# Kernel optimization log

Measured on AMD Instinct MI355X. Metric: run time of the kernel, lower is better.

## Reference

```python
import jax, jax.numpy as jnp
import numpy as np

D_MODEL = 1024
NUM_HEADS = 16
HEAD_DIM = D_MODEL // NUM_HEADS
BATCH = 2
SEQ = 2048


def setup_inputs() -> dict:
    key = jax.random.key(0)
    ks = jax.random.split(key, 9)
    s_in = 1.0 / np.sqrt(D_MODEL)  # kaiming-ish fan-in scaling for stability
    return {
        "x": jax.random.normal(ks[0], (BATCH, SEQ, D_MODEL), jnp.float32),
        "wq": jax.random.normal(ks[1], (D_MODEL, D_MODEL), jnp.float32) * s_in,
        "bq": jnp.zeros((D_MODEL,), jnp.float32),
        "wk": jax.random.normal(ks[2], (D_MODEL, D_MODEL), jnp.float32) * s_in,
        "bk": jnp.zeros((D_MODEL,), jnp.float32),
        "wv": jax.random.normal(ks[3], (D_MODEL, D_MODEL), jnp.float32) * s_in,
        "bv": jnp.zeros((D_MODEL,), jnp.float32),
        "wo": jax.random.normal(ks[4], (D_MODEL, D_MODEL), jnp.float32) * s_in,
        "bo": jnp.zeros((D_MODEL,), jnp.float32),
    }


def reference(x, wq, bq, wk, bk, wv, bv, wo, bo):
    B, S, _ = x.shape
    # QKV projections, split heads: [B, H, S, Dh]
    def proj(w, b):
        y = x @ w + b
        return y.reshape(B, S, NUM_HEADS, HEAD_DIM).transpose(0, 2, 1, 3)

    q = proj(wq, bq)
    k = proj(wk, bk)
    v = proj(wv, bv)

    scale = 1.0 / jnp.sqrt(jnp.float32(HEAD_DIM))
    scores = jnp.einsum("bhsd,bhtd->bhst", q, k) * scale  # [B,H,S,S]
    attn = jax.nn.softmax(scores, axis=-1)
    out = jnp.einsum("bhst,bhtd->bhsd", attn, v)  # [B,H,S,Dh]
    out = out.transpose(0, 2, 1, 3).reshape(B, S, D_MODEL)
    return out @ wo + bo
```

## Files before the change

kernel.cpp:

```cpp
#include <hip/hip_runtime.h>
#include <stdint.h>
#include <stddef.h>


typedef __attribute__((ext_vector_type(8))) short short8;
typedef __attribute__((ext_vector_type(4))) float f32x4;
typedef __attribute__((ext_vector_type(16))) float f32x16;
typedef __attribute__((ext_vector_type(4))) unsigned short u16x4;

#define MFMA16(a, b, c) __builtin_amdgcn_mfma_f32_16x16x32_bf16((a), (b), (c), 0, 0, 0)
#define MFMA32(a, b, c) __builtin_amdgcn_mfma_f32_32x32x16_bf16((a), (b), (c), 0, 0, 0)
#define AS1 __attribute__((address_space(1)))
#define AS3 __attribute__((address_space(3)))

__device__ __forceinline__ unsigned short f2bf(float f) {
  union { float f; unsigned u; } v; v.f = f;
  unsigned r = v.u + 0x7fffu + ((v.u >> 16) & 1u);
  return (unsigned short)(r >> 16);
}

__device__ __forceinline__ unsigned cvt_pk_bf16(float lo, float hi) {
  unsigned r;
  asm("v_cvt_pk_bf16_f32 %0, %1, %2" : "=v"(r) : "v"(lo), "v"(hi));
  return r;
}

__device__ __forceinline__ void pl32_swap(unsigned& a, unsigned& b) {
  asm volatile("v_permlane32_swap_b32 %0, %1" : "+v"(a), "+v"(b));
}

__device__ __forceinline__ short8 mk8(unsigned a, unsigned b, unsigned c, unsigned d) {
  union { unsigned u[4]; short8 s; } v;
  v.u[0] = a; v.u[1] = b; v.u[2] = c; v.u[3] = d;
  return v.s;
}

__global__ __launch_bounds__(256) void cast_x_kernel(const float* __restrict__ x,
                                                     unsigned short* __restrict__ xb) {
  int i = (blockIdx.x * 256 + threadIdx.x) * 4;
  float4 v = *reinterpret_cast<const float4*>(x + i);
  u16x4 o;
  o.x = f2bf(v.x); o.y = f2bf(v.y); o.z = f2bf(v.z); o.w = f2bf(v.w);
  *reinterpret_cast<u16x4*>(xb + i) = o;
}

__global__ __launch_bounds__(256) void prep_w_kernel(const float* __restrict__ wq,
                                                     const float* __restrict__ wk,
                                                     const float* __restrict__ wv,
                                                     const float* __restrict__ wo,
                                                     unsigned short* __restrict__ wt) {
  __shared__ unsigned short t_lds[32][33];
  int bid = blockIdx.x;
  int wsel = bid >> 10;
  int rem = bid & 1023;
  int kb = (rem >> 5) << 5;
  int nb = (rem & 31) << 5;
  const float* W = (wsel == 0) ? wq : (wsel == 1) ? wk : (wsel == 2) ? wv : wo;
  int t = threadIdx.x;
  int r = t >> 3, c = (t & 7) * 4;
  float4 v = *reinterpret_cast<const float4*>(W + (size_t)(kb + r) * 1024 + nb + c);
  t_lds[r][c + 0] = f2bf(v.x);
  t_lds[r][c + 1] = f2bf(v.y);
  t_lds[r][c + 2] = f2bf(v.z);
  t_lds[r][c + 3] = f2bf(v.w);
  __syncthreads();
  u16x4 o;
  o.x = t_lds[c + 0][r]; o.y = t_lds[c + 1][r];
  o.z = t_lds[c + 2][r]; o.w = t_lds[c + 3][r];
  *reinterpret_cast<u16x4*>(wt + (size_t)(wsel * 1024 + nb + r) * 1024 + kb + c) = o;
}

__global__ __launch_bounds__(256) void pack_bias_kernel(const float* __restrict__ bq,
                                                        const float* __restrict__ bk,
                                                        const float* __restrict__ bv,
                                                        float* __restrict__ bias3) {
  int i = blockIdx.x * 256 + threadIdx.x;
  if (i < 3072) bias3[i] = (i < 1024) ? bq[i] : (i < 2048) ? bk[i - 1024] : bv[i - 2048];
}

template <typename OutT, bool QS>
__global__ __launch_bounds__(256) void gemm_bt_kernel(const unsigned short* __restrict__ A,
                                                      const unsigned short* __restrict__ Bt,
                                                      const float* __restrict__ bias,
                                                      OutT* __restrict__ C, int N) {
  constexpr int K = 1024;
  __shared__ __align__(16) unsigned short a_lds[2][128 * 32];
  __shared__ __align__(16) unsigned short b_lds[2][128 * 32];
  const int nb = N >> 7;
  const int nwg = nb << 5;
  const int cpx = nwg >> 3;
  const int wg = ((int)blockIdx.x & 7) * cpx + ((int)blockIdx.x >> 3);
  const int bm = wg / nb;
  const int bn = wg % nb;
  const int m0 = bm << 7, n0 = bn << 7;
  const int tid = threadIdx.x;
  const int w = tid >> 6, l = tid & 63;
  const int lr = l & 15, lg = l >> 4;
  const int wm = (w >> 1) << 6, wn = (w & 1) << 6;

  const int q0 = w * 2, q1 = w * 2 + 1;
  const unsigned short* pa0 = A + (size_t)(m0 + q0 * 16 + (l >> 2)) * K + (l & 3) * 8;
  const unsigned short* pa1 = A + (size_t)(m0 + q1 * 16 + (l >> 2)) * K + (l & 3) * 8;
  const unsigned short* pb0 = Bt + (size_t)(n0 + q0 * 16 + (l >> 2)) * K + (l & 3) * 8;
  const unsigned short* pb1 = Bt + (size_t)(n0 + q1 * 16 + (l >> 2)) * K + (l & 3) * 8;

#define GEMM_STAGE(buf, k0)                                                        \
  do {                                                                             \
    __builtin_amdgcn_global_load_lds((const AS1 void*)(pa0 + (k0)),                \
        (AS3 void*)(&a_lds[buf][q0 * 512]), 16, 0, 0);                             \
    __builtin_amdgcn_global_load_lds((const AS1 void*)(pa1 + (k0)),                \
        (AS3 void*)(&a_lds[buf][q1 * 512]), 16, 0, 0);                             \
    __builtin_amdgcn_global_load_lds((const AS1 void*)(pb0 + (k0)),                \
        (AS3 void*)(&b_lds[buf][q0 * 512]), 16, 0, 0);                             \
    __builtin_amdgcn_global_load_lds((const AS1 void*)(pb1 + (k0)),                \
        (AS3 void*)(&b_lds[buf][q1 * 512]), 16, 0, 0);                             \
  } while (0)

  f32x4 acc[4][4] = {};
  GEMM_STAGE(0, 0);
  __syncthreads();

  int cur = 0;
  for (int k0 = 0; k0 < K; k0 += 32) {
    if (k0 + 32 < K) GEMM_STAGE(cur ^ 1, k0 + 32);
    short8 af[4], bfr[4];
#pragma unroll
    for (int i = 0; i < 4; ++i)
      af[i] = *reinterpret_cast<const short8*>(&a_lds[cur][(wm + i * 16 + lr) * 32 + lg * 8]);
#pragma unroll
    for (int i = 0; i < 4; ++i)
      bfr[i] = *reinterpret_cast<const short8*>(&b_lds[cur][(wn + i * 16 + lr) * 32 + lg * 8]);
#pragma unroll
    for (int i = 0; i < 4; ++i)
#pragma unroll
      for (int j = 0; j < 4; ++j)
        acc[i][j] = MFMA16(af[i], bfr[j], acc[i][j]);
    __syncthreads();
    cur ^= 1;
  }
#undef GEMM_STAGE

  const float scale = (QS && n0 < 1024) ? 0.18033688011111f : 1.0f;
#pragma unroll
  for (int i = 0; i < 4; ++i) {
#pragma unroll
    for (int j = 0; j < 4; ++j) {
#pragma unroll
      for (int r = 0; r < 4; ++r) {
        int m = m0 + wm + i * 16 + lg * 4 + r;
        int n = n0 + wn + j * 16 + lr;
        float val = (acc[i][j][r] + bias[n]) * scale;
        if constexpr (sizeof(OutT) == 2) {
          C[(size_t)m * N + n] = (OutT)f2bf(val);
        } else {
          C[(size_t)m * N + n] = val;
        }
      }
    }
  }
}

__global__ __launch_bounds__(256) void attn_kernel(const unsigned short* __restrict__ qkv,
                                                   unsigned short* __restrict__ aout) {
  __shared__ __align__(16) char lds[32768];
  const int tid = threadIdx.x;
  const int w = tid >> 6, l = tid & 63;
  const int lq = l & 31, hi = l >> 5;
  const int wg = ((int)blockIdx.x & 7) * 64 + ((int)blockIdx.x >> 3);
  const int qblk = wg & 15;
  const int bh = wg >> 4;
  const int b = bh >> 4, h = bh & 15;
  const size_t rowbase = (size_t)b * 2048;
  const int q0 = qblk * 128 + w * 32;

  short8 qf[4];
  {
    const unsigned short* qrow = qkv + (rowbase + q0 + lq) * 3072 + h * 64 + hi * 8;
#pragma unroll
    for (int c = 0; c < 4; ++c)
      qf[c] = *reinterpret_cast<const short8*>(qrow + c * 16);
  }

  const int r0 = 16 * w + (l >> 3);
  const int r1 = r0 + 8;
  const char* kq0_src = (const char*)(qkv + rowbase * 3072 + 1024 + h * 64) +
                        (size_t)r0 * 6144 + ((16 * (l & 7)) ^ ((r0 & 6) << 4));
  const char* kq1_src = (const char*)(qkv + rowbase * 3072 + 1024 + h * 64) +
                        (size_t)r1 * 6144 + ((16 * (l & 7)) ^ ((r1 & 6) << 4));
  const int kdst0 = 2 * w * 1024;
  const int kdst1 = kdst0 + 1024;

  const int pi = tid & 31;
  const int vd0 = (tid >> 5) * 8;
  const unsigned short* vptr_a = qkv + (rowbase + 2 * pi) * 3072 + 2048 + h * 64 + vd0;
  const unsigned short* vptr_b = vptr_a + 3072;

  int aoff[4];
#pragma unroll
  for (int c = 0; c < 4; ++c)
    aoff[c] = lq * 128 + ((c * 32 + hi * 16) ^ ((lq & 6) << 4));
  int vwoff[4];
#pragma unroll
  for (int jr = 0; jr < 4; ++jr)
    vwoff[jr] = 16384 + (vd0 + 2 * jr) * 128 + ((4 * pi) ^ ((2 * jr) << 4));

  float ls0 = 0.f, ls1 = 0.f, ls2 = 0.f, ls3 = 0.f;
  f32x16 ot0 = {}, ot1 = {};

  __builtin_amdgcn_global_load_lds((const AS1 void*)kq0_src, (AS3 void*)(lds + kdst0), 16, 0, 0);
  __builtin_amdgcn_global_load_lds((const AS1 void*)kq1_src, (AS3 void*)(lds + kdst1), 16, 0, 0);
  kq0_src += 393216; kq1_src += 393216;
  {
    short8 va = *reinterpret_cast<const short8*>(vptr_a);
    short8 vb = *reinterpret_cast<const short8*>(vptr_b);
    vptr_a += 64 * 3072; vptr_b += 64 * 3072;
    union { short8 s; unsigned u[4]; } ua, ub;
    ua.s = va; ub.s = vb;
#pragma unroll
    for (int jr = 0; jr < 4; ++jr) {
      unsigned w0 = __builtin_amdgcn_perm(ub.u[jr], ua.u[jr], 0x05040100u);
      unsigned w1 = __builtin_amdgcn_perm(ub.u[jr], ua.u[jr], 0x07060302u);
      *reinterpret_cast<unsigned*>(lds + vwoff[jr]) = w0;
      *reinterpret_cast<unsigned*>(lds + vwoff[jr] + 128) = w1;
    }
  }
  __syncthreads();

  int cur = 0;
  for (int t0 = 0; t0 < 2048; t0 += 64) {
    const bool more = (t0 + 64) < 2048;
    const int bmask = cur << 13;
    const int nmask = bmask ^ 8192;
    short8 va, vb;
    if (more) {
      __builtin_amdgcn_global_load_lds((const AS1 void*)kq0_src,
                                       (AS3 void*)(lds + nmask + kdst0), 16, 0, 0);
      __builtin_amdgcn_global_load_lds((const AS1 void*)kq1_src,
                                       (AS3 void*)(lds + nmask + kdst1), 16, 0, 0);
      kq0_src += 393216; kq1_src += 393216;
      va = *reinterpret_cast<const short8*>(vptr_a);
      vb = *reinterpret_cast<const short8*>(vptr_b);
      vptr_a += 64 * 3072; vptr_b += 64 * 3072;
    }

    const char* fb0 = lds + (aoff[0] ^ bmask);
    const char* fb1 = lds + (aoff[1] ^ bmask);
    const char* fb2 = lds + (aoff[2] ^ bmask);
    const char* fb3 = lds + (aoff[3] ^ bmask);

    f32x16 s0 = {}, s1 = {};
    __builtin_amdgcn_s_setprio(1);
    s0 = MFMA32(*reinterpret_cast<const short8*>(fb0), qf[0], s0);
    s1 = MFMA32(*reinterpret_cast<const short8*>(fb0 + 4096), qf[0], s1);
    s0 = MFMA32(*reinterpret_cast<const short8*>(fb1), qf[1], s0);
    s1 = MFMA32(*reinterpret_cast<const short8*>(fb1 + 4096), qf[1], s1);
    s0 = MFMA32(*reinterpret_cast<const short8*>(fb2), qf[2], s0);
    s1 = MFMA32(*reinterpret_cast<const short8*>(fb2 + 4096), qf[2], s1);
    s0 = MFMA32(*reinterpret_cast<const short8*>(fb3), qf[3], s0);
    s1 = MFMA32(*reinterpret_cast<const short8*>(fb3 + 4096), qf[3], s1);
    __builtin_amdgcn_s_setprio(0);

    if (more) {
      union { short8 s; unsigned u[4]; } ua, ub;
      ua.s = va; ub.s = vb;
#pragma unroll
      for (int jr = 0; jr < 4; ++jr) {
        unsigned w0 = __builtin_amdgcn_perm(ub.u[jr], ua.u[jr], 0x05040100u);
        unsigned w1 = __builtin_amdgcn_perm(ub.u[jr], ua.u[jr], 0x07060302u);
        *reinterpret_cast<unsigned*>(lds + (vwoff[jr] ^ nmask) - 16384 + 16384) = w0;
        *reinterpret_cast<unsigned*>(lds + (vwoff[jr] ^ nmask) + 128) = w1;
      }
    }

    float p0[16], p1[16];
#pragma unroll
    for (int i = 0; i < 16; ++i) {
      p0[i] = __builtin_exp2f(s0[i]);
      if ((i & 3) == 0) ls0 += p0[i]; else if ((i & 3) == 1) ls1 += p0[i];
      else if ((i & 3) == 2) ls2 += p0[i]; else ls3 += p0[i];
    }
#pragma unroll
    for (int i = 0; i < 16; ++i) {
      p1[i] = __builtin_exp2f(s1[i]);
      if ((i & 3) == 0) ls0 += p1[i]; else if ((i & 3) == 1) ls1 += p1[i];
      else if ((i & 3) == 2) ls2 += p1[i]; else ls3 += p1[i];
    }

    short8 pf[4];
    {
      unsigned a0 = cvt_pk_bf16(p0[0], p0[1]),   a1 = cvt_pk_bf16(p0[4], p0[5]);
      unsigned b0 = cvt_pk_bf16(p0[2], p0[3]),   b1 = cvt_pk_bf16(p0[6], p0[7]);
      pl32_swap(a0, a1); pl32_swap(b0, b1);
      pf[0] = mk8(a0, b0, a1, b1);
      unsigned c0 = cvt_pk_bf16(p0[8], p0[9]),   c1 = cvt_pk_bf16(p0[12], p0[13]);
      unsigned d0 = cvt_pk_bf16(p0[10], p0[11]), d1 = cvt_pk_bf16(p0[14], p0[15]);
      pl32_swap(c0, c1); pl32_swap(d0, d1);
      pf[1] = mk8(c0, d0, c1, d1);
      unsigned e0 = cvt_pk_bf16(p1[0], p1[1]),   e1 = cvt_pk_bf16(p1[4], p1[5]);
      unsigned f0 = cvt_pk_bf16(p1[2], p1[3]),   f1 = cvt_pk_bf16(p1[6], p1[7]);
      pl32_swap(e0, e1); pl32_swap(f0, f1);
      pf[2] = mk8(e0, f0, e1, f1);
      unsigned g0 = cvt_pk_bf16(p1[8], p1[9]),   g1 = cvt_pk_bf16(p1[12], p1[13]);
      unsigned h0 = cvt_pk_bf16(p1[10], p1[11]), h1 = cvt_pk_bf16(p1[14], p1[15]);
      pl32_swap(g0, g1); pl32_swap(h0, h1);
      pf[3] = mk8(g0, h0, g1, h1);
    }

    __builtin_amdgcn_s_setprio(1);
    ot0 = MFMA32(*reinterpret_cast<const short8*>(fb0 + 16384), pf[0], ot0);
    ot1 = MFMA32(*reinterpret_cast<const short8*>(fb0 + 20480), pf[0], ot1);
    ot0 = MFMA32(*reinterpret_cast<const short8*>(fb1 + 16384), pf[1], ot0);
    ot1 = MFMA32(*reinterpret_cast<const short8*>(fb1 + 20480), pf[1], ot1);
    ot0 = MFMA32(*reinterpret_cast<const short8*>(fb2 + 16384), pf[2], ot0);
    ot1 = MFMA32(*reinterpret_cast<const short8*>(fb2 + 20480), pf[2], ot1);
    ot0 = MFMA32(*reinterpret_cast<const short8*>(fb3 + 16384), pf[3], ot0);
    ot1 = MFMA32(*reinterpret_cast<const short8*>(fb3 + 20480), pf[3], ot1);
    __builtin_amdgcn_s_setprio(0);

    __syncthreads();
    cur ^= 1;
  }

  float lsum = (ls0 + ls1) + (ls2 + ls3);
  lsum += __shfl_xor(lsum, 32, 64);
  const float inv = 1.0f / lsum;
  char* ob = lds + w * 4096;
  const int swz_lq = (lq & 6) << 4;
#pragma unroll
  for (int r = 0; r < 16; r += 2) {
    int d = (r & 3) + 8 * (r >> 2) + 4 * hi;
    unsigned pk0 = cvt_pk_bf16(ot0[r] * inv, ot0[r + 1] * inv);
    *(unsigned*)(ob + lq * 128 + ((2 * d) ^ swz_lq)) = pk0;
    unsigned pk1 = cvt_pk_bf16(ot1[r] * inv, ot1[r + 1] * inv);
    *(unsigned*)(ob + lq * 128 + ((2 * (32 + d)) ^ swz_lq)) = pk1;
  }
  __syncthreads();
#pragma unroll
  for (int it = 0; it < 4; ++it) {
    int qq = it * 32 + (tid >> 3);
    int ch = tid & 7;
    const char* src = lds + (qq >> 5) * 4096;
    short8 vv = *reinterpret_cast<const short8*>(
        src + (qq & 31) * 128 + ((ch * 16) ^ (((qq & 31) & 6) << 4)));
    *reinterpret_cast<short8*>(aout + (rowbase + qblk * 128 + qq) * 1024 + h * 64 + ch * 8) = vv;
  }
}

extern "C" void kernel_launch(void* const* d_in, const int* in_sizes, int n_in,
                              void* d_out, int out_size, void* d_ws, size_t ws_size,
                              hipStream_t stream) {
  const float* x  = (const float*)d_in[0];
  const float* wq = (const float*)d_in[1];
  const float* bq = (const float*)d_in[2];
  const float* wk = (const float*)d_in[3];
  const float* bk = (const float*)d_in[4];
  const float* wv = (const float*)d_in[5];
  const float* bv = (const float*)d_in[6];
  const float* wo = (const float*)d_in[7];
  const float* bo = (const float*)d_in[8];
  float* out = (float*)d_out;

  char* ws = (char*)d_ws;
  unsigned short* xb    = (unsigned short*)(ws);
  unsigned short* aob   = (unsigned short*)(ws);
  unsigned short* wt    = (unsigned short*)(ws + 8388608);
  float*          bias3 = (float*)(ws + 16777216);
  unsigned short* qkvb  = (unsigned short*)(ws + 16777216 + 16384);

  cast_x_kernel<<<4096, 256, 0, stream>>>(x, xb);
  prep_w_kernel<<<4096, 256, 0, stream>>>(wq, wk, wv, wo, wt);
  pack_bias_kernel<<<12, 256, 0, stream>>>(bq, bk, bv, bias3);

  gemm_bt_kernel<unsigned short, true><<<768, 256, 0, stream>>>(xb, wt, bias3, qkvb, 3072);

  attn_kernel<<<512, 256, 0, stream>>>(qkvb, aob);

  gemm_bt_kernel<float, false><<<256, 256, 0, stream>>>(aob, wt + (size_t)3072 * 1024, bo, out, 1024);
}
```

Baseline: 141.3 us.

## Write V transposed from QKV GEMM and split attention keys across waves

The QKV projection epilogue now writes Q and K into a 2048-wide buffer and V in a pre-transposed [b,h,d,s] layout. This removes the in-kernel permute and LDS staging of V in attention. The attention kernel drops LDS double buffering and reads K and V fragments straight from global memory. It uses 128-thread blocks over 32 query rows, where each of the two waves handles half the keys, and merges the partial outputs and row sums through LDS at the end. The change aims for more parallelism and less LDS and sync traffic, at the cost of uncoalesced strided global loads of K and direct global V reads with no explicit prefetch.

```diff
diff --git a/kernel.cpp b/kernel.cpp
--- a/kernel.cpp
+++ b/kernel.cpp
@@ -78,11 +78,14 @@
   if (i < 3072) bias3[i] = (i < 1024) ? bq[i] : (i < 2048) ? bk[i - 1024] : bv[i - 2048];
 }
 
-template <typename OutT, bool QS>
+template <int MODE>
 __global__ __launch_bounds__(256) void gemm_bt_kernel(const unsigned short* __restrict__ A,
                                                       const unsigned short* __restrict__ Bt,
                                                       const float* __restrict__ bias,
-                                                      OutT* __restrict__ C, int N) {
+                                                      float* __restrict__ Cf,
+                                                      unsigned short* __restrict__ qk,
+                                                      unsigned short* __restrict__ vt,
+                                                      int N) {
   constexpr int K = 1024;
   __shared__ __align__(16) unsigned short a_lds[2][128 * 32];
   __shared__ __align__(16) unsigned short b_lds[2][128 * 32];
@@ -140,137 +143,94 @@
   }
 #undef GEMM_STAGE
 
-  const float scale = (QS && n0 < 1024) ? 0.18033688011111f : 1.0f;
-#pragma unroll
-  for (int i = 0; i < 4; ++i) {
-#pragma unroll
-    for (int j = 0; j < 4; ++j) {
-#pragma unroll
-      for (int r = 0; r < 4; ++r) {
-        int m = m0 + wm + i * 16 + lg * 4 + r;
-        int n = n0 + wn + j * 16 + lr;
-        float val = (acc[i][j][r] + bias[n]) * scale;
-        if constexpr (sizeof(OutT) == 2) {
-          C[(size_t)m * N + n] = (OutT)f2bf(val);
-        } else {
-          C[(size_t)m * N + n] = val;
+  if constexpr (MODE == 0) {
+#pragma unroll
+    for (int i = 0; i < 4; ++i)
+#pragma unroll
+      for (int j = 0; j < 4; ++j)
+#pragma unroll
+        for (int r = 0; r < 4; ++r) {
+          int m = m0 + wm + i * 16 + lg * 4 + r;
+          int n = n0 + wn + j * 16 + lr;
+          Cf[(size_t)m * N + n] = acc[i][j][r] + bias[n];
+        }
+  } else {
+    if (n0 < 2048) {
+      const float scale = (n0 < 1024) ? 0.18033688011111f : 1.0f;
+#pragma unroll
+      for (int i = 0; i < 4; ++i)
+#pragma unroll
+        for (int j = 0; j < 4; ++j)
+#pragma unroll
+          for (int r = 0; r < 4; ++r) {
+            int m = m0 + wm + i * 16 + lg * 4 + r;
+            int n = n0 + wn + j * 16 + lr;
+            qk[(size_t)m * 2048 + n] = f2bf((acc[i][j][r] + bias[n]) * scale);
+          }
+    } else {
+#pragma unroll
+      for (int i = 0; i < 4; ++i) {
+        int m_ = m0 + wm + i * 16 + lg * 4;
+        int bb = m_ >> 11, ss = m_ & 2047;
+#pragma unroll
+        for (int j = 0; j < 4; ++j) {
+          int np = n0 - 2048 + wn + j * 16 + lr;
+          int hh = np >> 6, dd = np & 63;
+          float bv = bias[np + 2048];
+          u16x4 pk;
+          pk.x = f2bf(acc[i][j][0] + bv);
+          pk.y = f2bf(acc[i][j][1] + bv);
+          pk.z = f2bf(acc[i][j][2] + bv);
+          pk.w = f2bf(acc[i][j][3] + bv);
+          *reinterpret_cast<u16x4*>(vt + (size_t)(bb * 16 + hh) * 131072 + dd * 2048 + ss) = pk;
         }
       }
     }
   }
 }
 
-__global__ __launch_bounds__(256) void attn_kernel(const unsigned short* __restrict__ qkv,
-                                                   unsigned short* __restrict__ aout) {
-  __shared__ __align__(16) char lds[32768];
+__global__ __launch_bounds__(128, 4) void attn_kernel(const unsigned short* __restrict__ qk,
+                                                      const unsigned short* __restrict__ vt,
+                                                      unsigned short* __restrict__ aout) {
+  __shared__ __align__(16) char lds[12544];
   const int tid = threadIdx.x;
   const int w = tid >> 6, l = tid & 63;
   const int lq = l & 31, hi = l >> 5;
-  const int wg = ((int)blockIdx.x & 7) * 64 + ((int)blockIdx.x >> 3);
-  const int qblk = wg & 15;
-  const int bh = wg >> 4;
+  const int wg = ((int)blockIdx.x & 7) * 256 + ((int)blockIdx.x >> 3);
+  const int bh = wg >> 6, qb = wg & 63;
   const int b = bh >> 4, h = bh & 15;
-  const size_t rowbase = (size_t)b * 2048;
-  const int q0 = qblk * 128 + w * 32;
 
   short8 qf[4];
   {
-    const unsigned short* qrow = qkv + (rowbase + q0 + lq) * 3072 + h * 64 + hi * 8;
+    const unsigned short* qrow = qk + (size_t)(b * 2048 + qb * 32 + lq) * 2048 + h * 64 + hi * 8;
 #pragma unroll
     for (int c = 0; c < 4; ++c)
       qf[c] = *reinterpret_cast<const short8*>(qrow + c * 16);
   }
 
-  const int r0 = 16 * w + (l >> 3);
-  const int r1 = r0 + 8;
-  const char* kq0_src = (const char*)(qkv + rowbase * 3072 + 1024 + h * 64) +
-                        (size_t)r0 * 6144 + ((16 * (l & 7)) ^ ((r0 & 6) << 4));
-  const char* kq1_src = (const char*)(qkv + rowbase * 3072 + 1024 + h * 64) +
-                        (size_t)r1 * 6144 + ((16 * (l & 7)) ^ ((r1 & 6) << 4));
-  const int kdst0 = 2 * w * 1024;
-  const int kdst1 = kdst0 + 1024;
-
-  const int pi = tid & 31;
-  const int vd0 = (tid >> 5) * 8;
-  const unsigned short* vptr_a = qkv + (rowbase + 2 * pi) * 3072 + 2048 + h * 64 + vd0;
-  const unsigned short* vptr_b = vptr_a + 3072;
-
-  int aoff[4];
-#pragma unroll
-  for (int c = 0; c < 4; ++c)
-    aoff[c] = lq * 128 + ((c * 32 + hi * 16) ^ ((lq & 6) << 4));
-  int vwoff[4];
-#pragma unroll
-  for (int jr = 0; jr < 4; ++jr)
-    vwoff[jr] = 16384 + (vd0 + 2 * jr) * 128 + ((4 * pi) ^ ((2 * jr) << 4));
+  const unsigned short* kp =
+      qk + (size_t)(b * 2048 + w * 1024 + lq) * 2048 + 1024 + h * 64 + hi * 8;
+  const unsigned short* vp = vt + (size_t)bh * 131072 + (size_t)lq * 2048 + w * 1024 + hi * 8;
 
   float ls0 = 0.f, ls1 = 0.f, ls2 = 0.f, ls3 = 0.f;
   f32x16 ot0 = {}, ot1 = {};
 
-  __builtin_amdgcn_global_load_lds((const AS1 void*)kq0_src, (AS3 void*)(lds + kdst0), 16, 0, 0);
-  __builtin_amdgcn_global_load_lds((const AS1 void*)kq1_src, (AS3 void*)(lds + kdst1), 16, 0, 0);
-  kq0_src += 393216; kq1_src += 393216;
-  {
-    short8 va = *reinterpret_cast<const short8*>(vptr_a);
-    short8 vb = *reinterpret_cast<const short8*>(vptr_b);
-    vptr_a += 64 * 3072; vptr_b += 64 * 3072;
-    union { short8 s; unsigned u[4]; } ua, ub;
-    ua.s = va; ub.s = vb;
-#pragma unroll
-    for (int jr = 0; jr < 4; ++jr) {
-      unsigned w0 = __builtin_amdgcn_perm(ub.u[jr], ua.u[jr], 0x05040100u);
-      unsigned w1 = __builtin_amdgcn_perm(ub.u[jr], ua.u[jr], 0x07060302u);
-      *reinterpret_cast<unsigned*>(lds + vwoff[jr]) = w0;
-      *reinterpret_cast<unsigned*>(lds + vwoff[jr] + 128) = w1;
-    }
-  }
-  __syncthreads();
-
-  int cur = 0;
-  for (int t0 = 0; t0 < 2048; t0 += 64) {
-    const bool more = (t0 + 64) < 2048;
-    const int bmask = cur << 13;
-    const int nmask = bmask ^ 8192;
-    short8 va, vb;
-    if (more) {
-      __builtin_amdgcn_global_load_lds((const AS1 void*)kq0_src,
-                                       (AS3 void*)(lds + nmask + kdst0), 16, 0, 0);
-      __builtin_amdgcn_global_load_lds((const AS1 void*)kq1_src,
-                                       (AS3 void*)(lds + nmask + kdst1), 16, 0, 0);
-      kq0_src += 393216; kq1_src += 393216;
-      va = *reinterpret_cast<const short8*>(vptr_a);
-      vb = *reinterpret_cast<const short8*>(vptr_b);
-      vptr_a += 64 * 3072; vptr_b += 64 * 3072;
-    }
-
-    const char* fb0 = lds + (aoff[0] ^ bmask);
-    const char* fb1 = lds + (aoff[1] ^ bmask);
-    const char* fb2 = lds + (aoff[2] ^ bmask);
-    const char* fb3 = lds + (aoff[3] ^ bmask);
+  for (int it = 0; it < 16; ++it) {
+    short8 vta[4];
+#pragma unroll
+    for (int c = 0; c < 4; ++c)
+      vta[c] = *reinterpret_cast<const short8*>(vp + c * 16);
 
     f32x16 s0 = {}, s1 = {};
     __builtin_amdgcn_s_setprio(1);
-    s0 = MFMA32(*reinterpret_cast<const short8*>(fb0), qf[0], s0);
-    s1 = MFMA32(*reinterpret_cast<const short8*>(fb0 + 4096), qf[0], s1);
-    s0 = MFMA32(*reinterpret_cast<const short8*>(fb1), qf[1], s0);
-    s1 = MFMA32(*reinterpret_cast<const short8*>(fb1 + 4096), qf[1], s1);
-    s0 = MFMA32(*reinterpret_cast<const short8*>(fb2), qf[2], s0);
-    s1 = MFMA32(*reinterpret_cast<const short8*>(fb2 + 4096), qf[2], s1);
-    s0 = MFMA32(*reinterpret_cast<const short8*>(fb3), qf[3], s0);
-    s1 = MFMA32(*reinterpret_cast<const short8*>(fb3 + 4096), qf[3], s1);
+#pragma unroll
+    for (int c = 0; c < 4; ++c) {
+      short8 kf0 = *reinterpret_cast<const short8*>(kp + c * 16);
+      short8 kf1 = *reinterpret_cast<const short8*>(kp + 32 * 2048 + c * 16);
+      s0 = MFMA32(kf0, qf[c], s0);
+      s1 = MFMA32(kf1, qf[c], s1);
+    }
     __builtin_amdgcn_s_setprio(0);
-
-    if (more) {
-      union { short8 s; unsigned u[4]; } ua, ub;
-      ua.s = va; ub.s = vb;
-#pragma unroll
-      for (int jr = 0; jr < 4; ++jr) {
-        unsigned w0 = __builtin_amdgcn_perm(ub.u[jr], ua.u[jr], 0x05040100u);
-        unsigned w1 = __builtin_amdgcn_perm(ub.u[jr], ua.u[jr], 0x07060302u);
-        *reinterpret_cast<unsigned*>(lds + (vwoff[jr] ^ nmask) - 16384 + 16384) = w0;
-        *reinterpret_cast<unsigned*>(lds + (vwoff[jr] ^ nmask) + 128) = w1;
-      }
-    }
 
     float p0[16], p1[16];
 #pragma unroll
@@ -307,42 +267,60 @@
     }
 
     __builtin_amdgcn_s_setprio(1);
-    ot0 = MFMA32(*reinterpret_cast<const short8*>(fb0 + 16384), pf[0], ot0);
-    ot1 = MFMA32(*reinterpret_cast<const short8*>(fb0 + 20480), pf[0], ot1);
-    ot0 = MFMA32(*reinterpret_cast<const short8*>(fb1 + 16384), pf[1], ot0);
-    ot1 = MFMA32(*reinterpret_cast<const short8*>(fb1 + 20480), pf[1], ot1);
-    ot0 = MFMA32(*reinterpret_cast<const short8*>(fb2 + 16384), pf[2], ot0);
-    ot1 = MFMA32(*reinterpret_cast<const short8*>(fb2 + 20480), pf[2], ot1);
-    ot0 = MFMA32(*reinterpret_cast<const short8*>(fb3 + 16384), pf[3], ot0);
-    ot1 = MFMA32(*reinterpret_cast<const short8*>(fb3 + 20480), pf[3], ot1);
+#pragma unroll
+    for (int c = 0; c < 4; ++c) {
+      short8 vtb = *reinterpret_cast<const short8*>(vp + 32 * 2048 + c * 16);
+      ot0 = MFMA32(vta[c], pf[c], ot0);
+      ot1 = MFMA32(vtb, pf[c], ot1);
+    }
     __builtin_amdgcn_s_setprio(0);
 
-    __syncthreads();
-    cur ^= 1;
-  }
+    kp += 64 * 2048;
+    vp += 64;
+  }
+
+  float* mbuf = (float*)lds;
+  float* dbuf = (float*)(lds + 8192);
+  char*  obuf = lds + 8320;
 
   float lsum = (ls0 + ls1) + (ls2 + ls3);
   lsum += __shfl_xor(lsum, 32, 64);
-  const float inv = 1.0f / lsum;
-  char* ob = lds + w * 4096;
-  const int swz_lq = (lq & 6) << 4;
-#pragma unroll
-  for (int r = 0; r < 16; r += 2) {
-    int d = (r & 3) + 8 * (r >> 2) + 4 * hi;
-    unsigned pk0 = cvt_pk_bf16(ot0[r] * inv, ot0[r + 1] * inv);
-    *(unsigned*)(ob + lq * 128 + ((2 * d) ^ swz_lq)) = pk0;
-    unsigned pk1 = cvt_pk_bf16(ot1[r] * inv, ot1[r + 1] * inv);
-    *(unsigned*)(ob + lq * 128 + ((2 * (32 + d)) ^ swz_lq)) = pk1;
+
+  if (w == 1) {
+#pragma unroll
+    for (int r = 0; r < 16; ++r) {
+      int d = (r & 3) + 8 * (r >> 2) + 4 * hi;
+      mbuf[d * 32 + lq] = ot0[r];
+      mbuf[(32 + d) * 32 + lq] = ot1[r];
+    }
+    if (hi == 0) dbuf[lq] = lsum;
   }
   __syncthreads();
-#pragma unroll
-  for (int it = 0; it < 4; ++it) {
-    int qq = it * 32 + (tid >> 3);
-    int ch = tid & 7;
-    const char* src = lds + (qq >> 5) * 4096;
-    short8 vv = *reinterpret_cast<const short8*>(
-        src + (qq & 31) * 128 + ((ch * 16) ^ (((qq & 31) & 6) << 4)));
-    *reinterpret_cast<short8*>(aout + (rowbase + qblk * 128 + qq) * 1024 + h * 64 + ch * 8) = vv;
+  if (w == 0) {
+    const float inv = 1.0f / (lsum + dbuf[lq]);
+    const int swz = (lq & 7) << 4;
+#pragma unroll
+    for (int r = 0; r < 16; r += 2) {
+      int d = (r & 3) + 8 * (r >> 2) + 4 * hi;
+      float o0a = (ot0[r] + mbuf[d * 32 + lq]) * inv;
+      float o0b = (ot0[r + 1] + mbuf[(d + 1) * 32 + lq]) * inv;
+      *(unsigned*)(obuf + lq * 128 + ((2 * d) ^ swz)) = cvt_pk_bf16(o0a, o0b);
+      float o1a = (ot1[r] + mbuf[(32 + d) * 32 + lq]) * inv;
+      float o1b = (ot1[r + 1] + mbuf[(33 + d) * 32 + lq]) * inv;
+      *(unsigned*)(obuf + lq * 128 + ((2 * (32 + d)) ^ swz)) = cvt_pk_bf16(o1a, o1b);
+    }
+  }
+  __syncthreads();
+  {
+    int row = tid >> 2;
+    int c2 = (tid & 3) * 2;
+    int swzr = (row & 7) << 4;
+    const char* src = obuf + row * 128;
+    short8 v0 = *reinterpret_cast<const short8*>(src + ((c2 * 16) ^ swzr));
+    short8 v1 = *reinterpret_cast<const short8*>(src + (((c2 + 1) * 16) ^ swzr));
+    unsigned short* orow = aout + (size_t)(b * 2048 + qb * 32 + row) * 1024 + h * 64 + c2 * 8;
+    *reinterpret_cast<short8*>(orow) = v0;
+    *reinterpret_cast<short8*>(orow + 8) = v1;
   }
 }
 
@@ -365,15 +343,17 @@
   unsigned short* aob   = (unsigned short*)(ws);
   unsigned short* wt    = (unsigned short*)(ws + 8388608);
   float*          bias3 = (float*)(ws + 16777216);
-  unsigned short* qkvb  = (unsigned short*)(ws + 16777216 + 16384);
+  unsigned short* qkb   = (unsigned short*)(ws + 16777216 + 16384);
+  unsigned short* vtb   = (unsigned short*)(ws + 33554432 + 16384);
 
   cast_x_kernel<<<4096, 256, 0, stream>>>(x, xb);
   prep_w_kernel<<<4096, 256, 0, stream>>>(wq, wk, wv, wo, wt);
   pack_bias_kernel<<<12, 256, 0, stream>>>(bq, bk, bv, bias3);
 
-  gemm_bt_kernel<unsigned short, true><<<768, 256, 0, stream>>>(xb, wt, bias3, qkvb, 3072);
-
-  attn_kernel<<<512, 256, 0, stream>>>(qkvb, aob);
-
-  gemm_bt_kernel<float, false><<<256, 256, 0, stream>>>(aob, wt + (size_t)3072 * 1024, bo, out, 1024);
-}
+  gemm_bt_kernel<1><<<768, 256, 0, stream>>>(xb, wt, bias3, nullptr, qkb, vtb, 3072);
+
+  attn_kernel<<<2048, 128, 0, stream>>>(qkb, vtb, aob);
+
+  gemm_bt_kernel<0><<<256, 256, 0, stream>>>(aob, wt + (size_t)3072 * 1024, bo, out,
+                                             nullptr, nullptr, 1024);
+}
```

Result: slower. 217.6 us (+54.0%).
